# Kernel tuning notes

Measured on AMD Instinct MI355X. Metric: run time of the kernel, lower is better.

## Reference

```python
import jax, jax.numpy as jnp
import numpy as np

B, C, H, W = 64, 1, 512, 512


def setup_inputs() -> dict:
    key = jax.random.key(0)
    k1, k2, k3, k4 = jax.random.split(key, 4)
    predict_cls = jax.random.uniform(k1, (B,), dtype=jnp.float32)          # probs in [0,1)
    predict_seg = jax.random.normal(k2, (B, C, H, W), dtype=jnp.float32)    # logits
    labels = jax.random.randint(k3, (B,), 0, 2, dtype=jnp.int32)            # {0,1}
    masks = jax.random.randint(k4, (B, C, H, W), 0, 2).astype(jnp.float32)  # binary gt
    return {"predict_cls": predict_cls, "predict_seg": predict_seg,
            "labels": labels, "masks": masks}


def reference(predict_cls, predict_seg, labels, masks):
    pc = predict_cls.astype(jnp.float32)
    ps = jax.nn.sigmoid(predict_seg.astype(jnp.float32))
    lab = labels.astype(jnp.float32)
    m = masks.astype(jnp.float32)

    # classification BCE (mean reduction, is_average=True)
    eps = 1e-7
    pc_c = jnp.clip(pc, eps, 1.0 - eps)
    cls_loss = -jnp.mean(lab * jnp.log(pc_c) + (1.0 - lab) * jnp.log(1.0 - pc_c))

    # segmentation dice over samples selected by predict_cls >= 0.5 (masked, vectorized)
    red_axes = tuple(range(1, ps.ndim))          # sum over (C,H,W) per sample
    pg = jnp.sum(ps * m, axis=red_axes)          # [B] intersection
    pp = jnp.sum(ps * ps, axis=red_axes)         # [B]
    gg = jnp.sum(m * m, axis=red_axes)           # [B]
    psum = jnp.sum(ps, axis=red_axes)            # [B]

    dice_pos = (2.0 * pg + 1e-5) / (pp + gg + 1e-5)   # label == 1
    dice_neg = 25.0 / (psum + 25.0)                    # label != 1
    dice = jnp.where(lab == 1.0, dice_pos, dice_neg)   # [B]

    sel = (pc >= 0.5).astype(jnp.float32)               # selected samples
    n = jnp.sum(sel)
    dice_sum = jnp.sum(sel * dice)
    seg_loss = jnp.where(n > 0.0,
                         (n - dice_sum) / jnp.maximum(n, 1.0),
                         jnp.float32(1e-4))             # fallback like tensor(0.0001)
    return (cls_loss, seg_loss)
```

## Files before the change

kernel.cpp:

```cpp
#include <hip/hip_runtime.h>

#define NSAMP 64
#define ELEMS (512 * 512)
#define NBLK  32
#define TPB   256

__global__ __launch_bounds__(TPB) void partials_kernel(
    const float* __restrict__ seg, const float* __restrict__ msk,
    float* __restrict__ ws)
{
    const int b    = blockIdx.x / NBLK;
    const int blk  = blockIdx.x % NBLK;
    const int per_block = ELEMS / NBLK;
    const size_t base = (size_t)b * ELEMS + (size_t)blk * per_block;
    const float4* s4 = (const float4*)(seg + base);
    const float4* m4 = (const float4*)(msk + base);
    const int n4 = per_block / 4;

    float pg = 0.f, pp = 0.f, gg = 0.f, sm = 0.f;

    for (int i = threadIdx.x; i < n4; i += TPB) {
        float4 x = s4[i];
        float4 m = m4[i];
        {
            float s = 1.0f / (1.0f + __expf(-x.x));
            pg = fmaf(s, m.x, pg); pp = fmaf(s, s, pp);
            gg = fmaf(m.x, m.x, gg); sm += s;
        }
        {
            float s = 1.0f / (1.0f + __expf(-x.y));
            pg = fmaf(s, m.y, pg); pp = fmaf(s, s, pp);
            gg = fmaf(m.y, m.y, gg); sm += s;
        }
        {
            float s = 1.0f / (1.0f + __expf(-x.z));
            pg = fmaf(s, m.z, pg); pp = fmaf(s, s, pp);
            gg = fmaf(m.z, m.z, gg); sm += s;
        }
        {
            float s = 1.0f / (1.0f + __expf(-x.w));
            pg = fmaf(s, m.w, pg); pp = fmaf(s, s, pp);
            gg = fmaf(m.w, m.w, gg); sm += s;
        }
    }

    #pragma unroll
    for (int o = 32; o; o >>= 1) {
        pg += __shfl_down(pg, o);
        pp += __shfl_down(pp, o);
        gg += __shfl_down(gg, o);
        sm += __shfl_down(sm, o);
    }

    __shared__ float red[TPB / 64][4];
    const int lane = threadIdx.x & 63;
    const int wid  = threadIdx.x >> 6;
    if (lane == 0) {
        red[wid][0] = pg; red[wid][1] = pp;
        red[wid][2] = gg; red[wid][3] = sm;
    }
    __syncthreads();
    if (threadIdx.x == 0) {
        float a = 0.f, c = 0.f, d = 0.f, e = 0.f;
        #pragma unroll
        for (int w = 0; w < TPB / 64; ++w) {
            a += red[w][0]; c += red[w][1];
            d += red[w][2]; e += red[w][3];
        }
        float* o = ws + (size_t)blockIdx.x * 4;
        o[0] = a; o[1] = c; o[2] = d; o[3] = e;
    }
}

__global__ __launch_bounds__(64) void final_kernel(
    const float* __restrict__ pc, const int* __restrict__ labels,
    const float* __restrict__ ws, float* __restrict__ out)
{
    const int b = threadIdx.x;

    float pg = 0.f, pp = 0.f, gg = 0.f, sm = 0.f;
    for (int i = 0; i < NBLK; ++i) {
        const float* w = ws + ((size_t)b * NBLK + i) * 4;
        pg += w[0]; pp += w[1]; gg += w[2]; sm += w[3];
    }

    float p   = pc[b];
    float lab = (float)labels[b];

    const float eps = 1e-7f;
    float pcc = fminf(fmaxf(p, eps), 1.f - eps);
    float bce = -(lab * logf(pcc) + (1.f - lab) * logf(1.f - pcc));

    float dice_pos = (2.f * pg + 1e-5f) / (pp + gg + 1e-5f);
    float dice_neg = 25.f / (sm + 25.f);
    float dice = (lab == 1.f) ? dice_pos : dice_neg;

    float sel  = (p >= 0.5f) ? 1.f : 0.f;
    float nsel = sel;
    float dsum = sel * dice;

    #pragma unroll
    for (int o = 32; o; o >>= 1) {
        bce  += __shfl_down(bce, o);
        nsel += __shfl_down(nsel, o);
        dsum += __shfl_down(dsum, o);
    }

    if (b == 0) {
        out[0] = bce * (1.0f / 64.0f);
        out[1] = (nsel > 0.f) ? (nsel - dsum) / fmaxf(nsel, 1.f) : 1e-4f;
    }
}

extern "C" void kernel_launch(void* const* d_in, const int* in_sizes, int n_in,
                              void* d_out, int out_size, void* d_ws, size_t ws_size,
                              hipStream_t stream) {
    const float* predict_cls = (const float*)d_in[0];
    const float* predict_seg = (const float*)d_in[1];
    const int*   labels      = (const int*)d_in[2];
    const float* masks       = (const float*)d_in[3];
    float* out = (float*)d_out;
    float* ws  = (float*)d_ws;

    partials_kernel<<<NSAMP * NBLK, TPB, 0, stream>>>(predict_seg, masks, ws);
    final_kernel<<<1, 64, 0, stream>>>(predict_cls, labels, ws, out);
}
```

Baseline: 28.42 us.

## Double block count, fully unroll loads up front, use fast rcp sigmoid

Raises the per-sample block split from 32 to 64, so each thread issues all of its float4 loads (4 seg + 4 mask) before any compute, giving more memory-level parallelism. Sigmoid now uses the hardware reciprocal instead of a full divide, and gg is computed as a plain sum because the mask is binary. The final kernel now reduces twice as many partials using 256 threads with float4 reads. This costs more registers per thread, a larger workspace, and slightly less precise sigmoid values.

```diff
diff --git a/kernel.cpp b/kernel.cpp
--- a/kernel.cpp
+++ b/kernel.cpp
@@ -2,46 +2,47 @@
 
 #define NSAMP 64
 #define ELEMS (512 * 512)
-#define NBLK  32
+#define NBLK  64
 #define TPB   256
+#define PB    (ELEMS / NBLK)
+#define N4    (PB / 4)
+#define UNR   (N4 / TPB)
+
+__device__ __forceinline__ float sigmoid_fast(float x) {
+    float e = __expf(-x);
+    return __builtin_amdgcn_rcpf(1.0f + e);
+}
 
 __global__ __launch_bounds__(TPB) void partials_kernel(
     const float* __restrict__ seg, const float* __restrict__ msk,
     float* __restrict__ ws)
 {
-    const int b    = blockIdx.x / NBLK;
-    const int blk  = blockIdx.x % NBLK;
-    const int per_block = ELEMS / NBLK;
-    const size_t base = (size_t)b * ELEMS + (size_t)blk * per_block;
+    const int b   = blockIdx.x >> 6;
+    const int blk = blockIdx.x & (NBLK - 1);
+    const size_t base = (size_t)b * ELEMS + (size_t)blk * PB;
     const float4* s4 = (const float4*)(seg + base);
     const float4* m4 = (const float4*)(msk + base);
-    const int n4 = per_block / 4;
+
+    float4 xs[UNR], ms[UNR];
+    #pragma unroll
+    for (int u = 0; u < UNR; ++u) xs[u] = s4[threadIdx.x + u * TPB];
+    #pragma unroll
+    for (int u = 0; u < UNR; ++u) ms[u] = m4[threadIdx.x + u * TPB];
 
     float pg = 0.f, pp = 0.f, gg = 0.f, sm = 0.f;
-
-    for (int i = threadIdx.x; i < n4; i += TPB) {
-        float4 x = s4[i];
-        float4 m = m4[i];
-        {
-            float s = 1.0f / (1.0f + __expf(-x.x));
-            pg = fmaf(s, m.x, pg); pp = fmaf(s, s, pp);
-            gg = fmaf(m.x, m.x, gg); sm += s;
-        }
-        {
-            float s = 1.0f / (1.0f + __expf(-x.y));
-            pg = fmaf(s, m.y, pg); pp = fmaf(s, s, pp);
-            gg = fmaf(m.y, m.y, gg); sm += s;
-        }
-        {
-            float s = 1.0f / (1.0f + __expf(-x.z));
-            pg = fmaf(s, m.z, pg); pp = fmaf(s, s, pp);
-            gg = fmaf(m.z, m.z, gg); sm += s;
-        }
-        {
-            float s = 1.0f / (1.0f + __expf(-x.w));
-            pg = fmaf(s, m.w, pg); pp = fmaf(s, s, pp);
-            gg = fmaf(m.w, m.w, gg); sm += s;
-        }
+    #pragma unroll
+    for (int u = 0; u < UNR; ++u) {
+        float4 x = xs[u], m = ms[u];
+        float s0 = sigmoid_fast(x.x);
+        float s1 = sigmoid_fast(x.y);
+        float s2 = sigmoid_fast(x.z);
+        float s3 = sigmoid_fast(x.w);
+        pg = fmaf(s0, m.x, pg); pg = fmaf(s1, m.y, pg);
+        pg = fmaf(s2, m.z, pg); pg = fmaf(s3, m.w, pg);
+        pp = fmaf(s0, s0, pp);  pp = fmaf(s1, s1, pp);
+        pp = fmaf(s2, s2, pp);  pp = fmaf(s3, s3, pp);
+        gg += (m.x + m.y) + (m.z + m.w);
+        sm += (s0 + s1) + (s2 + s3);
     }
 
     #pragma unroll
@@ -61,54 +62,67 @@
     }
     __syncthreads();
     if (threadIdx.x == 0) {
-        float a = 0.f, c = 0.f, d = 0.f, e = 0.f;
-        #pragma unroll
-        for (int w = 0; w < TPB / 64; ++w) {
-            a += red[w][0]; c += red[w][1];
-            d += red[w][2]; e += red[w][3];
-        }
-        float* o = ws + (size_t)blockIdx.x * 4;
-        o[0] = a; o[1] = c; o[2] = d; o[3] = e;
+        float a = red[0][0] + red[1][0] + red[2][0] + red[3][0];
+        float c = red[0][1] + red[1][1] + red[2][1] + red[3][1];
+        float d = red[0][2] + red[1][2] + red[2][2] + red[3][2];
+        float e = red[0][3] + red[1][3] + red[2][3] + red[3][3];
+        ((float4*)ws)[blockIdx.x] = make_float4(a, c, d, e);
     }
 }
 
-__global__ __launch_bounds__(64) void final_kernel(
+__global__ __launch_bounds__(256) void final_kernel(
     const float* __restrict__ pc, const int* __restrict__ labels,
     const float* __restrict__ ws, float* __restrict__ out)
 {
-    const int b = threadIdx.x;
+    const int t = threadIdx.x;
+    const int b = t & 63;
+    const int q = t >> 6;
+    const float4* w4 = (const float4*)ws;
 
-    float pg = 0.f, pp = 0.f, gg = 0.f, sm = 0.f;
-    for (int i = 0; i < NBLK; ++i) {
-        const float* w = ws + ((size_t)b * NBLK + i) * 4;
-        pg += w[0]; pp += w[1]; gg += w[2]; sm += w[3];
+    float4 acc = make_float4(0.f, 0.f, 0.f, 0.f);
+    #pragma unroll
+    for (int i = 0; i < NBLK / 4; ++i) {
+        float4 v = w4[(size_t)b * NBLK + q * (NBLK / 4) + i];
+        acc.x += v.x; acc.y += v.y; acc.z += v.z; acc.w += v.w;
     }
 
-    float p   = pc[b];
-    float lab = (float)labels[b];
+    __shared__ float4 red[256];
+    red[t] = acc;
+    __syncthreads();
 
-    const float eps = 1e-7f;
-    float pcc = fminf(fmaxf(p, eps), 1.f - eps);
-    float bce = -(lab * logf(pcc) + (1.f - lab) * logf(1.f - pcc));
+    if (t < 64) {
+        float4 a0 = red[t], a1 = red[t + 64], a2 = red[t + 128], a3 = red[t + 192];
+        float pg = (a0.x + a1.x) + (a2.x + a3.x);
+        float pp = (a0.y + a1.y) + (a2.y + a3.y);
+        float gg = (a0.z + a1.z) + (a2.z + a3.z);
+        float sm = (a0.w + a1.w) + (a2.w + a3.w);
 
-    float dice_pos = (2.f * pg + 1e-5f) / (pp + gg + 1e-5f);
-    float dice_neg = 25.f / (sm + 25.f);
-    float dice = (lab == 1.f) ? dice_pos : dice_neg;
+        float p   = pc[b];
+        float lab = (float)labels[b];
 
-    float sel  = (p >= 0.5f) ? 1.f : 0.f;
-    float nsel = sel;
-    float dsum = sel * dice;
+        const float eps = 1e-7f;
+        float pcc = fminf(fmaxf(p, eps), 1.f - eps);
+        float bce = -(lab * logf(pcc) + (1.f - lab) * logf(1.f - pcc));
 
-    #pragma unroll
-    for (int o = 32; o; o >>= 1) {
-        bce  += __shfl_down(bce, o);
-        nsel += __shfl_down(nsel, o);
-        dsum += __shfl_down(dsum, o);
-    }
+        float dice_pos = (2.f * pg + 1e-5f) / (pp + gg + 1e-5f);
+        float dice_neg = 25.f / (sm + 25.f);
+        float dice = (lab == 1.f) ? dice_pos : dice_neg;
 
-    if (b == 0) {
-        out[0] = bce * (1.0f / 64.0f);
-        out[1] = (nsel > 0.f) ? (nsel - dsum) / fmaxf(nsel, 1.f) : 1e-4f;
+        float sel  = (p >= 0.5f) ? 1.f : 0.f;
+        float nsel = sel;
+        float dsum = sel * dice;
+
+        #pragma unroll
+        for (int o = 32; o; o >>= 1) {
+            bce  += __shfl_down(bce, o);
+            nsel += __shfl_down(nsel, o);
+            dsum += __shfl_down(dsum, o);
+        }
+
+        if (b == 0) {
+            out[0] = bce * (1.0f / 64.0f);
+            out[1] = (nsel > 0.f) ? (nsel - dsum) / fmaxf(nsel, 1.f) : 1e-4f;
+        }
     }
 }
 
@@ -123,5 +137,5 @@
     float* ws  = (float*)d_ws;
 
     partials_kernel<<<NSAMP * NBLK, TPB, 0, stream>>>(predict_seg, masks, ws);
-    final_kernel<<<1, 64, 0, stream>>>(predict_cls, labels, ws, out);
+    final_kernel<<<1, 256, 0, stream>>>(predict_cls, labels, ws, out);
 }
```

Measured after the change: 28.75 us. Within noise of the previous version (+1.2%).
